# Optimization experiments

Measured on AMD Instinct MI355X. Metric: run time of the kernel, lower is better.

## Reference

```python
import jax, jax.numpy as jnp
import numpy as np
import math

N_HEAD = 16
D_MODEL = 1024
ATT_DIM = D_MODEL // N_HEAD


def setup_inputs() -> dict:
    key = jax.random.key(0)
    ks = jax.random.split(key, 11)
    B, T, D = 2, 2048, D_MODEL
    s = 1.0 / math.sqrt(D)
    return {
        "q": jax.random.normal(ks[0], (B, T, D), jnp.float32),
        "k": jax.random.normal(ks[1], (B, T, D), jnp.float32),
        "v": jax.random.normal(ks[2], (B, T, D), jnp.float32),
        "Wq": jax.random.normal(ks[3], (D, D), jnp.float32) * s,
        "bq": jnp.zeros((D,), jnp.float32),
        "Wk": jax.random.normal(ks[4], (D, D), jnp.float32) * s,
        "bk": jnp.zeros((D,), jnp.float32),
        "Wv": jax.random.normal(ks[5], (D, D), jnp.float32) * s,
        "bv": jnp.zeros((D,), jnp.float32),
        "Wo": jax.random.normal(ks[6], (D, D), jnp.float32) * s,
        "bo": jnp.zeros((D,), jnp.float32),
    }


def reference(q, k, v, Wq, bq, Wk, bk, Wv, bv, Wo, bo):
    B, T, D = q.shape
    H, hd = N_HEAD, ATT_DIM
    # Linear projections (torch Linear: x @ W.T + b)
    qh = (q @ Wq.T + bq).reshape(B, T, H, hd).transpose(0, 2, 1, 3)  # [B,H,T,hd]
    kh = (k @ Wk.T + bk).reshape(B, T, H, hd).transpose(0, 2, 1, 3)
    vh = (v @ Wv.T + bv).reshape(B, T, H, hd).transpose(0, 2, 1, 3)
    scale = 1.0 / math.sqrt(hd)
    score = jnp.einsum("bhqd,bhkd->bhqk", qh, kh) * scale  # [B,H,T,T]
    attn = jax.nn.softmax(score, axis=-1)
    out = jnp.einsum("bhqk,bhkd->bhqd", attn, vh)  # [B,H,T,hd]
    out = out.transpose(0, 2, 1, 3).reshape(B, T, D)
    return out @ Wo.T + bo
```

## Files before the change

### kernel.cpp

```cpp
#include <hip/hip_runtime.h>


typedef __attribute__((ext_vector_type(8))) short bf16x8;
typedef __attribute__((ext_vector_type(4))) float f32x4;
typedef __attribute__((ext_vector_type(4))) unsigned int u32x4;

#define E22 ((size_t)1 << 22)
#define E20 ((size_t)1 << 20)

__device__ __forceinline__ unsigned short f2bf(float x) {
    unsigned int u = __float_as_uint(x);
    u += 0x7fffu + ((u >> 16) & 1u);
    return (unsigned short)(u >> 16);
}
__device__ __forceinline__ unsigned int pk2bf(float a, float b) {
    return __builtin_amdgcn_perm(__float_as_uint(a), __float_as_uint(b), 0x03020706u);
}
__device__ __forceinline__ void gl16(const void* g, void* l) {
    __builtin_amdgcn_global_load_lds(
        (const __attribute__((address_space(1))) void*)g,
        (__attribute__((address_space(3))) void*)l, 16, 0, 0);
}
__device__ __forceinline__ f32x4 mfma16(bf16x8 a, bf16x8 b, f32x4 c) {
    return __builtin_amdgcn_mfma_f32_16x16x32_bf16(a, b, c, 0, 0, 0);
}

__global__ __launch_bounds__(256)
void split_all(const float* __restrict__ q, const float* __restrict__ k,
               const float* __restrict__ v, const float* __restrict__ wq,
               const float* __restrict__ wk, const float* __restrict__ wv,
               const float* __restrict__ wo, unsigned short* __restrict__ ws)
{
    const size_t t = (size_t)blockIdx.x * 256 + threadIdx.x;
    const size_t e = t * 4;
    const float* src; unsigned short* dst; size_t off;
    if (e < 3 * E22) {
        const unsigned int which = (unsigned int)(e >> 22);
        src = which == 0 ? q : (which == 1 ? k : v);
        off = e & (E22 - 1);
        dst = ws + (size_t)which * E22;
    } else {
        const size_t e2 = e - 3 * E22;
        const unsigned int which = (unsigned int)(e2 >> 20);
        off = e2 & (E20 - 1);
        src = which == 0 ? wq : (which == 1 ? wk : (which == 2 ? wv : wo));
        dst = ws + 3 * E22 + (size_t)which * E20;
    }
    const float4 xv = *(const float4*)(src + off);
    ushort4 h4;
    h4.x = f2bf(xv.x); h4.y = f2bf(xv.y); h4.z = f2bf(xv.z); h4.w = f2bf(xv.w);
    *(ushort4*)(dst + off) = h4;
}

__global__ __launch_bounds__(256)
void gemm_qkv(const unsigned short* __restrict__ Xall,
              const unsigned short* __restrict__ Wcat,
              const float* __restrict__ bq, const float* __restrict__ bk,
              const float* __restrict__ bv, unsigned short* __restrict__ Qhp,
              unsigned short* __restrict__ Khp, unsigned short* __restrict__ Vtp)
{
    __shared__ unsigned short Xs[3 * 4096], Ws[3 * 4096];
    const int tid = threadIdx.x;
    const int w = tid >> 6, ln = tid & 63;
    const int quad = ln >> 4, L = ln & 15;
    const int wy = w >> 1, wx = w & 1;

    const int bid = blockIdx.x;
    const int xcd = bid & 7, j = bid >> 3;
    const int gg = xcd * 12 + (j >> 3);
    const int which = gg >> 5, m_i = gg & 31, n_i = j & 7;
    const int m0 = m_i * 128;

    const unsigned short* X = Xall + (size_t)which * E22;
    const unsigned short* W = Wcat + ((size_t)which * 1024 + n_i * 128) * 1024;
    const float* bp = which == 0 ? bq : (which == 1 ? bk : bv);
    unsigned short* outp = which == 0 ? Qhp : (which == 1 ? Khp : Vtp);
    const float qscale = which == 0 ? 0.18033688011f : 1.0f;

    const int ci0 = ln, ci1 = 64 + ln;
    const int row0 = w * 32 + (ci0 >> 2), row1 = w * 32 + (ci1 >> 2);
    const int gc0 = (ci0 & 3) ^ ((row0 >> 1) & 3);
    const int gc1 = (ci1 & 3) ^ ((row1 >> 1) & 3);
    const int lb0 = w * 2048, lb1 = w * 2048 + 1024;
    const unsigned short* Xbp = X + (size_t)m0 * 1024;
    const size_t gx0 = (size_t)row0 * 1024 + gc0 * 8;
    const size_t gx1 = (size_t)row1 * 1024 + gc1 * 8;

    f32x4 acc[4][4];
#pragma unroll
    for (int i = 0; i < 4; ++i)
#pragma unroll
        for (int jj = 0; jj < 4; ++jj) { f32x4 z = {0.f,0.f,0.f,0.f}; acc[i][jj] = z; }

#define QSTAGE(k0_, bo_)                                                       \
    do {                                                                       \
        gl16(Xbp + gx0 + (k0_), (char*)Xs + (bo_) + lb0);                      \
        gl16(W   + gx0 + (k0_), (char*)Ws + (bo_) + lb0);                      \
        gl16(Xbp + gx1 + (k0_), (char*)Xs + (bo_) + lb1);                      \
        gl16(W   + gx1 + (k0_), (char*)Ws + (bo_) + lb1);                      \
    } while (0)

#define QCOMP(eo_)                                                             \
    do {                                                                       \
        const unsigned short* Xc = Xs + (eo_);                                 \
        const unsigned short* Wc = Ws + (eo_);                                 \
        bf16x8 ah[4], bh[4];                                                   \
        _Pragma("unroll")                                                      \
        for (int mt = 0; mt < 4; ++mt) {                                       \
            const int row = wy * 64 + mt * 16 + L;                             \
            ah[mt] = *(const bf16x8*)(Xc + row * 32 +                          \
                                      ((quad ^ ((row >> 1) & 3)) * 8));        \
        }                                                                      \
        _Pragma("unroll")                                                      \
        for (int nt = 0; nt < 4; ++nt) {                                       \
            const int row = wx * 64 + nt * 16 + L;                             \
            bh[nt] = *(const bf16x8*)(Wc + row * 32 +                          \
                                      ((quad ^ ((row >> 1) & 3)) * 8));        \
        }                                                                      \
        _Pragma("unroll")                                                      \
        for (int mt = 0; mt < 4; ++mt)                                         \
            _Pragma("unroll")                                                  \
            for (int nt = 0; nt < 4; ++nt)                                     \
                acc[mt][nt] = mfma16(ah[mt], bh[nt], acc[mt][nt]);             \
    } while (0)

    QSTAGE(0, 0);
    QSTAGE(32, 8192);

    int cur = 0;
    for (int kt = 0; kt < 31; ++kt) {
        asm volatile("s_waitcnt vmcnt(4)" ::: "memory");
        __builtin_amdgcn_s_barrier();
        asm volatile("" ::: "memory");
        if (kt < 30) {
            int st = cur + 2; if (st >= 3) st -= 3;
            QSTAGE((kt + 2) * 32, st * 8192);
        }
        QCOMP(cur * 4096);
        cur = (cur == 2) ? 0 : cur + 1;
    }
    asm volatile("s_waitcnt vmcnt(0)" ::: "memory");
    __builtin_amdgcn_s_barrier();
    asm volatile("" ::: "memory");
    QCOMP(cur * 4096);
#undef QSTAGE
#undef QCOMP

#pragma unroll
    for (int mt = 0; mt < 4; ++mt)
#pragma unroll
        for (int nt = 0; nt < 4; ++nt) {
            const int gm0 = m0 + wy * 64 + mt * 16 + quad * 4;
            const int bn  = n_i * 128 + wx * 64 + nt * 16 + L;
            const float bvv = bp[bn];
            const int hh = bn >> 6, dd = bn & 63;
            if (which < 2) {
#pragma unroll
                for (int r = 0; r < 4; ++r) {
                    const int gm = gm0 + r;
                    const int bb = gm >> 11, tt = gm & 2047;
                    outp[((size_t)(bb * 16 + hh) * 2048 + tt) * 64 + dd] =
                        f2bf((acc[mt][nt][r] + bvv) * qscale);
                }
            } else {
                const int bb = gm0 >> 11, t0 = gm0 & 2047;
                const int c5 = t0 & 31;
                const int p0 = (t0 & ~31) | (((c5 & 15) >> 2) << 3) | ((c5 >> 4) << 2);
                ushort4 pk;
                pk.x = f2bf(acc[mt][nt][0] + bvv);
                pk.y = f2bf(acc[mt][nt][1] + bvv);
                pk.z = f2bf(acc[mt][nt][2] + bvv);
                pk.w = f2bf(acc[mt][nt][3] + bvv);
                *(ushort4*)(outp + ((size_t)(bb * 16 + hh) * 64 + dd) * 2048 + p0) = pk;
            }
        }
}

__global__ __launch_bounds__(256)
void gemm_out(const unsigned short* __restrict__ X, const unsigned short* __restrict__ W,
              const float* __restrict__ bias, float* __restrict__ outp)
{
    __shared__ unsigned short Xs[4 * 4096], Ws[4 * 2048];
    const int tid = threadIdx.x;
    const int w = tid >> 6, ln = tid & 63;
    const int quad = ln >> 4, L = ln & 15;

    const int bid = blockIdx.x;
    const int xcd = bid & 7, j = bid >> 3;
    const int m0 = (xcd * 4 + (j >> 4)) * 128;
    const int n0 = (j & 15) * 64;

    const int cix0 = ln, cix1 = 64 + ln;
    const int rowx0 = w * 32 + (cix0 >> 2), rowx1 = w * 32 + (cix1 >> 2);
    const int gcx0 = (cix0 & 3) ^ ((rowx0 >> 1) & 3);
    const int gcx1 = (cix1 & 3) ^ ((rowx1 >> 1) & 3);
    const int roww = w * 16 + (ln >> 2);
    const int gcw = (ln & 3) ^ ((roww >> 1) & 3);
    const size_t gxx0 = (size_t)(m0 + rowx0) * 1024 + gcx0 * 8;
    const size_t gxx1 = (size_t)(m0 + rowx1) * 1024 + gcx1 * 8;
    const size_t gww  = (size_t)(n0 + roww) * 1024 + gcw * 8;

    f32x4 acc[2][4];
#pragma unroll
    for (int i = 0; i < 2; ++i)
#pragma unroll
        for (int jj = 0; jj < 4; ++jj) { f32x4 z = {0.f,0.f,0.f,0.f}; acc[i][jj] = z; }

#define OSTAGE(kt_, bs_)                                                       \
    do {                                                                       \
        gl16(X + gxx0 + (kt_) * 32, (char*)Xs + (bs_) * 8192 + w * 2048);      \
        gl16(X + gxx1 + (kt_) * 32, (char*)Xs + (bs_) * 8192 + w * 2048 + 1024); \
        gl16(W + gww  + (kt_) * 32, (char*)Ws + (bs_) * 4096 + w * 1024);      \
    } while (0)

#define OCOMP(bs_)                                                             \
    do {                                                                       \
        const unsigned short* Xc = Xs + (bs_) * 4096;                          \
        const unsigned short* Wc = Ws + (bs_) * 2048;                          \
        bf16x8 ah[2], bh[4];                                                   \
        _Pragma("unroll")                                                      \
        for (int mt = 0; mt < 2; ++mt) {                                       \
            const int row = w * 32 + mt * 16 + L;                              \
            ah[mt] = *(const bf16x8*)(Xc + row * 32 +                          \
                                      ((quad ^ ((row >> 1) & 3)) * 8));        \
        }                                                                      \
        _Pragma("unroll")                                                      \
        for (int nt = 0; nt < 4; ++nt) {                                       \
            const int row = nt * 16 + L;                                       \
            bh[nt] = *(const bf16x8*)(Wc + row * 32 +                          \
                                      ((quad ^ ((row >> 1) & 3)) * 8));        \
        }                                                                      \
        _Pragma("unroll")                                                      \
        for (int mt = 0; mt < 2; ++mt)                                         \
            _Pragma("unroll")                                                  \
            for (int nt = 0; nt < 4; ++nt)                                     \
                acc[mt][nt] = mfma16(ah[mt], bh[nt], acc[mt][nt]);             \
    } while (0)

    OSTAGE(0, 0);
    OSTAGE(1, 1);

    for (int p = 0; p < 16; ++p) {
        const int c2 = (p & 1) * 2;
        __syncthreads();
        if (p < 15) {
            OSTAGE(2 * p + 2, c2 ^ 2);
            OSTAGE(2 * p + 3, (c2 ^ 2) + 1);
        }
        OCOMP(c2);
        OCOMP(c2 + 1);
    }
#undef OSTAGE
#undef OCOMP

#pragma unroll
    for (int mt = 0; mt < 2; ++mt)
#pragma unroll
        for (int nt = 0; nt < 4; ++nt) {
            const int gm0 = m0 + w * 32 + mt * 16 + quad * 4;
            const int gn  = n0 + nt * 16 + L;
            const float bvv = bias[gn];
#pragma unroll
            for (int r = 0; r < 4; ++r)
                outp[(size_t)(gm0 + r) * 1024 + gn] = acc[mt][nt][r] + bvv;
        }
}

__global__ __launch_bounds__(256, 2)
void flash(const unsigned short* __restrict__ Qh, const unsigned short* __restrict__ Kh,
           const unsigned short* __restrict__ Vt, unsigned short* __restrict__ A)
{
    __shared__ unsigned short SM[32768];
    __shared__ float Lsc[2 * 4 * 64];
    const int tid = threadIdx.x;
    const int w = tid >> 6, ln = tid & 63;
    const int quad = ln >> 4, L = ln & 15;
    const int wq = w & 1, wk = w >> 1;

    const int bid = blockIdx.x;
    const int xcd = bid & 7, j = bid >> 3;
    const int bh_i = xcd * 4 + (j & 3);
    const int qt = j >> 2;
    const int b = bh_i >> 4, h = bh_i & 15;

    const unsigned short* Qb = Qh + ((size_t)bh_i * 2048 + qt * 128 + wq * 64) * 64;
    const unsigned short* Kb = Kh + (size_t)bh_i * 2048 * 64;
    const unsigned short* Vb = Vt + (size_t)bh_i * 64 * 2048;

    bf16x8 bq[4][2];
#pragma unroll
    for (int nt = 0; nt < 4; ++nt)
#pragma unroll
        for (int kc = 0; kc < 2; ++kc)
            bq[nt][kc] = *(const bf16x8*)(Qb + (nt * 16 + L) * 64 + kc * 32 + quad * 8);

    const short one_bf = (short)0x3F80;
    bf16x8 bone = {one_bf, one_bf, one_bf, one_bf, one_bf, one_bf, one_bf, one_bf};

    f32x4 o[4][4];
    f32x4 lacc[4];
#pragma unroll
    for (int mtd = 0; mtd < 4; ++mtd)
#pragma unroll
        for (int nt = 0; nt < 4; ++nt) { f32x4 z = {0.f,0.f,0.f,0.f}; o[mtd][nt] = z; }
#pragma unroll
    for (int nt = 0; nt < 4; ++nt) { f32x4 z = {0.f,0.f,0.f,0.f}; lacc[nt] = z; }

    const int ci0 = (w * 2 + 0) * 64 + ln, ci1 = (w * 2 + 1) * 64 + ln;
    const int rr0 = ci0 >> 3, rr1 = ci1 >> 3;
    const int gc0 = (ci0 & 7) ^ (rr0 & 7), gc1 = (ci1 & 7) ^ (rr1 & 7);

#define STAGE1(kt_, b_, s_)                                                     \
    do {                                                                        \
        gl16(Kb + (size_t)((kt_) * 64 + rr0) * 64 + gc0 * 8,                    \
             (char*)SM + (b_) * 16384 + (s_) * 8192 + (w * 2 + 0) * 1024);      \
        gl16(Kb + (size_t)((kt_) * 64 + rr1) * 64 + gc1 * 8,                    \
             (char*)SM + (b_) * 16384 + (s_) * 8192 + (w * 2 + 1) * 1024);      \
        gl16(Vb + (size_t)rr0 * 2048 + (kt_) * 64 + gc0 * 8,                    \
             (char*)SM + 32768 + (b_) * 16384 + (s_) * 8192 + (w * 2 + 0) * 1024); \
        gl16(Vb + (size_t)rr1 * 2048 + (kt_) * 64 + gc1 * 8,                    \
             (char*)SM + 32768 + (b_) * 16384 + (s_) * 8192 + (w * 2 + 1) * 1024); \
    } while (0)

#define SUBCOMP(b_, s_)                                                         \
    do {                                                                        \
        const unsigned short* Ksb = SM + (b_) * 8192 + (s_) * 4096;             \
        const unsigned short* Vsb = SM + 16384 + (b_) * 8192 + (s_) * 4096;     \
        bf16x8 ak[2][2];                                                        \
        _Pragma("unroll")                                                       \
        for (int mt = 0; mt < 2; ++mt)                                          \
            _Pragma("unroll")                                                   \
            for (int kc = 0; kc < 2; ++kc) {                                    \
                const int row = wk * 32 + mt * 16 + L;                          \
                ak[mt][kc] = *(const bf16x8*)(Ksb + row * 64 +                  \
                                              (((kc * 4 + quad) ^ (L & 7)) * 8)); \
            }                                                                   \
        f32x4 s[2][4];                                                          \
        _Pragma("unroll")                                                       \
        for (int mt = 0; mt < 2; ++mt)                                          \
            _Pragma("unroll")                                                   \
            for (int nt = 0; nt < 4; ++nt) {                                    \
                f32x4 z = {0.f, 0.f, 0.f, 0.f};                                 \
                z = mfma16(ak[mt][0], bq[nt][0], z);                            \
                z = mfma16(ak[mt][1], bq[nt][1], z);                            \
                s[mt][nt] = z;                                                  \
            }                                                                   \
        bf16x8 pbx[4];                                                          \
        _Pragma("unroll")                                                       \
        for (int nt = 0; nt < 4; ++nt) {                                        \
            u32x4 pd;                                                           \
            pd.x = pk2bf(__builtin_amdgcn_exp2f(s[0][nt][0]),                   \
                         __builtin_amdgcn_exp2f(s[0][nt][1]));                  \
            pd.y = pk2bf(__builtin_amdgcn_exp2f(s[0][nt][2]),                   \
                         __builtin_amdgcn_exp2f(s[0][nt][3]));                  \
            pd.z = pk2bf(__builtin_amdgcn_exp2f(s[1][nt][0]),                   \
                         __builtin_amdgcn_exp2f(s[1][nt][1]));                  \
            pd.w = pk2bf(__builtin_amdgcn_exp2f(s[1][nt][2]),                   \
                         __builtin_amdgcn_exp2f(s[1][nt][3]));                  \
            pbx[nt] = __builtin_bit_cast(bf16x8, pd);                           \
        }                                                                       \
        bf16x8 av[4];                                                           \
        _Pragma("unroll")                                                       \
        for (int mtd = 0; mtd < 4; ++mtd) {                                     \
            const int row = mtd * 16 + L;                                       \
            av[mtd] = *(const bf16x8*)(Vsb + row * 64 +                         \
                                       (((wk * 4 + quad) ^ (L & 7)) * 8));      \
        }                                                                       \
        _Pragma("unroll")                                                       \
        for (int mtd = 0; mtd < 4; ++mtd)                                       \
            _Pragma("unroll")                                                   \
            for (int nt = 0; nt < 4; ++nt)                                      \
                o[mtd][nt] = mfma16(av[mtd], pbx[nt], o[mtd][nt]);              \
        _Pragma("unroll")                                                       \
        for (int nt = 0; nt < 4; ++nt)                                          \
            lacc[nt] = mfma16(bone, pbx[nt], lacc[nt]);                         \
    } while (0)

    STAGE1(0, 0, 0);
    STAGE1(1, 0, 1);

    for (int p = 0; p < 16; ++p) {
        const int cur = p & 1;
        __syncthreads();
        if (p < 15) {
            STAGE1(2 * p + 2, cur ^ 1, 0);
            STAGE1(2 * p + 3, cur ^ 1, 1);
        }
        SUBCOMP(cur, 0);
        SUBCOMP(cur, 1);
    }
#undef STAGE1
#undef SUBCOMP

    __syncthreads();
    float* Rb = (float*)SM;
    if (wk == 1) {
#pragma unroll
        for (int mtd = 0; mtd < 4; ++mtd)
#pragma unroll
            for (int nt = 0; nt < 4; ++nt)
                *(f32x4*)(Rb + wq * 4096 + (mtd * 4 + nt) * 256 + ln * 4) = o[mtd][nt];
#pragma unroll
        for (int nt = 0; nt < 4; ++nt)
            Lsc[wq * 256 + nt * 64 + ln] = lacc[nt][0];
    }
    __syncthreads();
    if (wk == 0) {
#pragma unroll
        for (int mtd = 0; mtd < 4; ++mtd)
#pragma unroll
            for (int nt = 0; nt < 4; ++nt)
                o[mtd][nt] += *(const f32x4*)(Rb + wq * 4096 + (mtd * 4 + nt) * 256 + ln * 4);

#pragma unroll
        for (int nt = 0; nt < 4; ++nt) {
            const float lsum = lacc[nt][0] + Lsc[wq * 256 + nt * 64 + ln];
            const float inv = 1.0f / lsum;
            const int qrow = b * 2048 + qt * 128 + wq * 64 + nt * 16 + L;
#pragma unroll
            for (int mtd = 0; mtd < 4; ++mtd) {
                const int d0 = mtd * 16 + quad * 4;
                ushort4 pk;
                pk.x = f2bf(o[mtd][nt][0] * inv);
                pk.y = f2bf(o[mtd][nt][1] * inv);
                pk.z = f2bf(o[mtd][nt][2] * inv);
                pk.w = f2bf(o[mtd][nt][3] * inv);
                *(ushort4*)(A + (size_t)qrow * 1024 + h * 64 + d0) = pk;
            }
        }
    }
}

extern "C" void kernel_launch(void* const* d_in, const int* in_sizes, int n_in,
                              void* d_out, int out_size, void* d_ws, size_t ws_size,
                              hipStream_t stream) {
    const float* q  = (const float*)d_in[0];
    const float* k  = (const float*)d_in[1];
    const float* v  = (const float*)d_in[2];
    const float* Wq = (const float*)d_in[3];
    const float* bq = (const float*)d_in[4];
    const float* Wk = (const float*)d_in[5];
    const float* bk = (const float*)d_in[6];
    const float* Wv = (const float*)d_in[7];
    const float* bv = (const float*)d_in[8];
    const float* Wo = (const float*)d_in[9];
    const float* bo = (const float*)d_in[10];

    unsigned short* W = (unsigned short*)d_ws;
    unsigned short *Xall = W;
    unsigned short *Wcat = W + 3 * E22;
    unsigned short *Wob  = Wcat + 3 * E20;
    unsigned short *Qhp  = W + 4 * E22;
    unsigned short *Khp  = W + 5 * E22;
    unsigned short *Vtp  = W + 6 * E22;
    unsigned short *A    = W;

    split_all<<<16384, 256, 0, stream>>>(q, k, v, Wq, Wk, Wv, Wo, W);

    gemm_qkv<<<768, 256, 0, stream>>>(Xall, Wcat, bq, bk, bv, Qhp, Khp, Vtp);

    flash<<<512, 256, 0, stream>>>(Qhp, Khp, Vtp, A);

    gemm_out<<<512, 256, 0, stream>>>(A, Wob, bo, (float*)d_out);
}
```

Before: 209.1 us.

## Deepen gemm_out pipeline to triple buffering and widen split_all per-thread work

The output-projection GEMM moves from double-buffered pairs of k-tiles to a six-slot ring with two pairs in flight. It replaces __syncthreads with an explicit vmcnt wait plus barrier, so global-to-LDS loads for stage p+2 overlap compute on stage p. The fp32-to-bf16 conversion kernel now handles 8 elements per thread with half the blocks, which cuts launch and indexing overhead. The larger LDS footprint may reduce occupancy, and the hand-written vmcnt counting must match the loads actually issued.

```diff
diff --git a/kernel.cpp b/kernel.cpp
--- a/kernel.cpp
+++ b/kernel.cpp
@@ -32,7 +32,7 @@
                const float* __restrict__ wo, unsigned short* __restrict__ ws)
 {
     const size_t t = (size_t)blockIdx.x * 256 + threadIdx.x;
-    const size_t e = t * 4;
+    const size_t e = t * 8;
     const float* src; unsigned short* dst; size_t off;
     if (e < 3 * E22) {
         const unsigned int which = (unsigned int)(e >> 22);
@@ -46,10 +46,13 @@
         src = which == 0 ? wq : (which == 1 ? wk : (which == 2 ? wv : wo));
         dst = ws + 3 * E22 + (size_t)which * E20;
     }
-    const float4 xv = *(const float4*)(src + off);
-    ushort4 h4;
-    h4.x = f2bf(xv.x); h4.y = f2bf(xv.y); h4.z = f2bf(xv.z); h4.w = f2bf(xv.w);
-    *(ushort4*)(dst + off) = h4;
+    const float4 xa = *(const float4*)(src + off);
+    const float4 xb = *(const float4*)(src + off + 4);
+    ushort4 ha, hb;
+    ha.x = f2bf(xa.x); ha.y = f2bf(xa.y); ha.z = f2bf(xa.z); ha.w = f2bf(xa.w);
+    hb.x = f2bf(xb.x); hb.y = f2bf(xb.y); hb.z = f2bf(xb.z); hb.w = f2bf(xb.w);
+    *(ushort4*)(dst + off) = ha;
+    *(ushort4*)(dst + off + 4) = hb;
 }
 
 __global__ __launch_bounds__(256)
@@ -180,7 +183,7 @@
 void gemm_out(const unsigned short* __restrict__ X, const unsigned short* __restrict__ W,
               const float* __restrict__ bias, float* __restrict__ outp)
 {
-    __shared__ unsigned short Xs[4 * 4096], Ws[4 * 2048];
+    __shared__ unsigned short Xs[6 * 4096], Ws[6 * 2048];
     const int tid = threadIdx.x;
     const int w = tid >> 6, ln = tid & 63;
     const int quad = ln >> 4, L = ln & 15;
@@ -206,17 +209,17 @@
 #pragma unroll
         for (int jj = 0; jj < 4; ++jj) { f32x4 z = {0.f,0.f,0.f,0.f}; acc[i][jj] = z; }
 
-#define OSTAGE(kt_, bs_)                                                       \
+#define OSTAGE(kt_, sb_)                                                       \
     do {                                                                       \
-        gl16(X + gxx0 + (kt_) * 32, (char*)Xs + (bs_) * 8192 + w * 2048);      \
-        gl16(X + gxx1 + (kt_) * 32, (char*)Xs + (bs_) * 8192 + w * 2048 + 1024); \
-        gl16(W + gww  + (kt_) * 32, (char*)Ws + (bs_) * 4096 + w * 1024);      \
-    } while (0)
-
-#define OCOMP(bs_)                                                             \
+        gl16(X + gxx0 + (kt_) * 32, (char*)Xs + (sb_) * 8192 + w * 2048);      \
+        gl16(X + gxx1 + (kt_) * 32, (char*)Xs + (sb_) * 8192 + w * 2048 + 1024); \
+        gl16(W + gww  + (kt_) * 32, (char*)Ws + (sb_) * 4096 + w * 1024);      \
+    } while (0)
+
+#define OCOMP(sb_)                                                             \
     do {                                                                       \
-        const unsigned short* Xc = Xs + (bs_) * 4096;                          \
-        const unsigned short* Wc = Ws + (bs_) * 2048;                          \
+        const unsigned short* Xc = Xs + (sb_) * 4096;                          \
+        const unsigned short* Wc = Ws + (sb_) * 2048;                          \
         bf16x8 ah[2], bh[4];                                                   \
         _Pragma("unroll")                                                      \
         for (int mt = 0; mt < 2; ++mt) {                                       \
@@ -237,18 +240,25 @@
                 acc[mt][nt] = mfma16(ah[mt], bh[nt], acc[mt][nt]);             \
     } while (0)
 
-    OSTAGE(0, 0);
-    OSTAGE(1, 1);
+    OSTAGE(0, 0); OSTAGE(1, 1);
+    OSTAGE(2, 2); OSTAGE(3, 3);
 
     for (int p = 0; p < 16; ++p) {
-        const int c2 = (p & 1) * 2;
-        __syncthreads();
         if (p < 15) {
-            OSTAGE(2 * p + 2, c2 ^ 2);
-            OSTAGE(2 * p + 3, (c2 ^ 2) + 1);
-        }
-        OCOMP(c2);
-        OCOMP(c2 + 1);
+            asm volatile("s_waitcnt vmcnt(6)" ::: "memory");
+        } else {
+            asm volatile("s_waitcnt vmcnt(0)" ::: "memory");
+        }
+        __builtin_amdgcn_s_barrier();
+        asm volatile("" ::: "memory");
+        const int sb = (2 * p) % 6;
+        if (p < 14) {
+            const int st = (2 * p + 4) % 6;
+            OSTAGE(2 * p + 4, st);
+            OSTAGE(2 * p + 5, st + 1);
+        }
+        OCOMP(sb);
+        OCOMP(sb + 1);
     }
 #undef OSTAGE
 #undef OCOMP
@@ -455,7 +465,7 @@
     unsigned short *Vtp  = W + 6 * E22;
     unsigned short *A    = W;
 
-    split_all<<<16384, 256, 0, stream>>>(q, k, v, Wq, Wk, Wv, Wo, W);
+    split_all<<<8192, 256, 0, stream>>>(q, k, v, Wq, Wk, Wv, Wo, W);
 
     gemm_qkv<<<768, 256, 0, stream>>>(Xall, Wcat, bq, bk, bv, Qhp, Khp, Vtp);
 
```

Result: no change. 207.5 us (median of 2 runs) (-0.8%).
